# Kernel optimization log

Measured on AMD Instinct MI355X. Metric: run time of the kernel, lower is better.

Reference implementation:

```python
import jax, jax.numpy as jnp
import numpy as np

CROP = 20
HALF = CROP // 2  # also the zero-padding width
HID = 128
NCLS = 10
B = 16384


def setup_inputs() -> dict:
    key = jax.random.key(0)
    ks = jax.random.split(key, 16)
    s = 0.05
    inp = {
        "image": jax.random.uniform(ks[0], (B, 1, 28, 28), dtype=jnp.float32),
        # centers in padded coordinates, kept in-bounds: [HALF, 48-HALF]
        "center": jax.random.randint(ks[1], (B, 2), HALF, 48 - HALF + 1, dtype=jnp.int64),
        "h0": jax.random.normal(ks[2], (2, B, HID), dtype=jnp.float32),
        # RNN layer 0 (input 400 -> 128)
        "W_ih0": jax.random.normal(ks[3], (HID, CROP * CROP), dtype=jnp.float32) * s,
        "b_ih0": jax.random.normal(ks[4], (HID,), dtype=jnp.float32) * s,
        "W_hh0": jax.random.normal(ks[5], (HID, HID), dtype=jnp.float32) * s,
        "b_hh0": jax.random.normal(ks[6], (HID,), dtype=jnp.float32) * s,
        # RNN layer 1 (128 -> 128)
        "W_ih1": jax.random.normal(ks[7], (HID, HID), dtype=jnp.float32) * s,
        "b_ih1": jax.random.normal(ks[8], (HID,), dtype=jnp.float32) * s,
        "W_hh1": jax.random.normal(ks[9], (HID, HID), dtype=jnp.float32) * s,
        "b_hh1": jax.random.normal(ks[10], (HID,), dtype=jnp.float32) * s,
        # heads
        "W_cls": jax.random.normal(ks[11], (NCLS, HID), dtype=jnp.float32) * s,
        "b_cls": jax.random.normal(ks[12], (NCLS,), dtype=jnp.float32) * s,
        "W_act": jax.random.normal(ks[13], (2, HID), dtype=jnp.float32) * s,
        "b_act": jax.random.normal(ks[14], (2,), dtype=jnp.float32) * s,
    }
    return inp


def _crop(padded, center):
    # padded: (B,1,P,P), center: (B,2) with (x, y) in padded coords
    b = padded.shape[0]
    r = jnp.arange(CROP)
    ys = (center[:, 1] - HALF)[:, None] + r  # (B, CROP)
    xs = (center[:, 0] - HALF)[:, None] + r  # (B, CROP)
    bi = jnp.arange(b)[:, None, None]
    return padded[bi, 0, ys[:, :, None], xs[:, None, :]]  # (B, CROP, CROP)


def reference(image, center, h0,
              W_ih0, b_ih0, W_hh0, b_hh0,
              W_ih1, b_ih1, W_hh1, b_hh1,
              W_cls, b_cls, W_act, b_act):
    b = image.shape[0]
    padded = jnp.pad(image, ((0, 0), (0, 0), (HALF, HALF), (HALF, HALF)))
    x = _crop(padded, center).reshape(b, -1)  # (B, 400)
    # single-step, 2-layer tanh RNN
    h1 = jnp.tanh(x @ W_ih0.T + b_ih0 + h0[0] @ W_hh0.T + b_hh0)
    h2 = jnp.tanh(h1 @ W_ih1.T + b_ih1 + h0[1] @ W_hh1.T + b_hh1)
    hn = jnp.stack([h1, h2])  # (2, B, HID)
    class_pred = h2 @ W_cls.T + b_cls
    action_pred = h2 @ W_act.T + b_act
    return class_pred, action_pred, hn
```

## Files before the change

### kernel.cpp

```cpp
#include <hip/hip_runtime.h>
#include <hip/hip_bf16.h>

#define B_TOT 16384
#define MTILE 16

typedef __bf16 bf16x8 __attribute__((ext_vector_type(8)));
typedef float  f32x4  __attribute__((ext_vector_type(4)));

#define NG0 (17*8*64)
#define NG1 (8*8*64)
#define NGH (4*64)
#define WP0_OFF  0
#define WP1_OFF  (NG0*16)
#define WPH_OFF  (WP1_OFF + NG1*16)
#define BIAS0_OFF (WPH_OFF + NGH*16)
#define BIAS1_OFF (BIAS0_OFF + 512)
#define BIASH_OFF (BIAS1_OFF + 512)
#define PREP_BLOCKS 53

__device__ __forceinline__ float fast_tanh(float x) {
    float cx = fminf(fmaxf(x, -9.f), 9.f);
    float t = __builtin_amdgcn_exp2f(cx * 2.8853900817779268f);
    return 1.f - 2.f * __builtin_amdgcn_rcpf(t + 1.f);
}

__device__ __forceinline__ void gl_lds16(const void* g, void* l) {
    __builtin_amdgcn_global_load_lds((const __attribute__((address_space(1))) void*)g,
                                     (__attribute__((address_space(3))) void*)l, 16, 0, 0);
}

__device__ __forceinline__ bf16x8 cvt8(f32x4 a, f32x4 b) {
    bf16x8 v;
    v[0]=(__bf16)a.x; v[1]=(__bf16)a.y; v[2]=(__bf16)a.z; v[3]=(__bf16)a.w;
    v[4]=(__bf16)b.x; v[5]=(__bf16)b.y; v[6]=(__bf16)b.z; v[7]=(__bf16)b.w;
    return v;
}

__global__ __launch_bounds__(256) void prepack_kernel(
    const float* __restrict__ Wih0, const float* __restrict__ Whh0,
    const float* __restrict__ Wih1, const float* __restrict__ Whh1,
    const float* __restrict__ Wcls, const float* __restrict__ Wact,
    const float* __restrict__ bih0, const float* __restrict__ bhh0,
    const float* __restrict__ bih1, const float* __restrict__ bhh1,
    const float* __restrict__ bcls, const float* __restrict__ bact,
    char* __restrict__ ws)
{
    int idx = blockIdx.x * 256 + threadIdx.x;
    __bf16* wp0 = (__bf16*)(ws + WP0_OFF);
    __bf16* wp1 = (__bf16*)(ws + WP1_OFF);
    __bf16* wph = (__bf16*)(ws + WPH_OFF);
    float* bias0 = (float*)(ws + BIAS0_OFF);
    float* bias1 = (float*)(ws + BIAS1_OFF);
    float* biash = (float*)(ws + BIASH_OFF);

    if (idx < NG0) {
        int lane = idx & 63, g = idx >> 6, s = g >> 3, nb = g & 7;
        int n = nb * 16 + (lane & 15);
        int kb = s * 32 + (lane >> 4) * 8;
        bf16x8 v;
        #pragma unroll
        for (int j = 0; j < 8; ++j) {
            int k = kb + j;
            float x = 0.f;
            if (k < 400)       x = Wih0[n * 400 + k];
            else if (k >= 416) x = Whh0[n * 128 + (k - 416)];
            v[j] = (__bf16)x;
        }
        *(bf16x8*)(wp0 + (size_t)idx * 8) = v;
    } else if (idx < NG0 + NG1) {
        int i2 = idx - NG0;
        int lane = i2 & 63, g = i2 >> 6, s = g >> 3, nb = g & 7;
        int n = nb * 16 + (lane & 15);
        int kb = s * 32 + (lane >> 4) * 8;
        bf16x8 v;
        #pragma unroll
        for (int j = 0; j < 8; ++j) {
            int k = kb + j;
            float x = (k < 128) ? Wih1[n * 128 + k] : Whh1[n * 128 + (k - 128)];
            v[j] = (__bf16)x;
        }
        *(bf16x8*)(wp1 + (size_t)i2 * 8) = v;
    } else if (idx < NG0 + NG1 + NGH) {
        int i3 = idx - NG0 - NG1;
        int lane = i3 & 63, s = i3 >> 6;
        int n = lane & 15;
        int kb = s * 32 + (lane >> 4) * 8;
        bf16x8 v;
        #pragma unroll
        for (int j = 0; j < 8; ++j) {
            int k = kb + j;
            float x = 0.f;
            if (n < 10)      x = Wcls[n * 128 + k];
            else if (n < 12) x = Wact[(n - 10) * 128 + k];
            v[j] = (__bf16)x;
        }
        *(bf16x8*)(wph + (size_t)i3 * 8) = v;
    } else {
        int i4 = idx - NG0 - NG1 - NGH;
        if (i4 < 128) bias0[i4] = bih0[i4] + bhh0[i4];
        else if (i4 < 256) { int i = i4 - 128; bias1[i] = bih1[i] + bhh1[i]; }
        else if (i4 < 272) {
            int i = i4 - 256;
            biash[i] = (i < 10) ? bcls[i] : ((i < 12) ? bact[i - 10] : 0.f);
        }
    }
}

#define RAWW  560
#define XLSTR 424
#define HEXSTR 136

__global__ __launch_bounds__(256) void fused_main(
    const float* __restrict__ image, const int* __restrict__ center,
    const float* __restrict__ h0, const char* __restrict__ ws,
    float* __restrict__ out)
{
    const bf16x8* wp0 = (const bf16x8*)(ws + WP0_OFF);
    const bf16x8* wp1 = (const bf16x8*)(ws + WP1_OFF);
    const bf16x8* wph = (const bf16x8*)(ws + WPH_OFF);
    const float* bias0 = (const float*)(ws + BIAS0_OFF);
    const float* bias1 = (const float*)(ws + BIAS1_OFF);
    const float* biash = (const float*)(ws + BIASH_OFF);

    __shared__ __align__(16) float raw[MTILE * RAWW];
    __shared__ __align__(16) __bf16 stage[MTILE * XLSTR];
    __shared__ __align__(16) float h0st[8 * 256];
    __bf16* h1ex = (__bf16*)raw;
    __bf16* h2ex = (__bf16*)(raw + 2048);
    float*  h0st1 = raw + 4096;

    const int t = threadIdx.x, lane = t & 63, wn = t >> 6;
    const int m0 = blockIdx.x * MTILE;
    const int l15 = lane & 15, l16 = lane >> 4;

    #pragma unroll
    for (int u = 0; u < 2; ++u) {
        int c = wn * 2 + u;
        int s = c >> 1, half = c & 1;
        const float* src = h0 + (size_t)(m0 + l15) * 128 + s * 32 + l16 * 8 + half * 4;
        gl_lds16(src, &h0st[c * 256]);
    }

    {
        unsigned basel = lane * 16u;
        #pragma unroll
        for (int j = 0; j < 9; ++j) {
            int ii = wn + j * 4;
            if (ii < 35) {
                unsigned off = (unsigned)ii * 1024u + basel;
                unsigned sm = off / 2240u;
                unsigned within = off - sm * 2240u;
                int cyl = center[(m0 + sm) * 2 + 1];
                int rst = min(max(cyl - 20, 0), 8);
                const char* src = (const char*)image
                                + (size_t)(m0 + sm) * 3136 + (size_t)rst * 112 + within;
                gl_lds16(src, (char*)raw + (size_t)ii * 1024);
            }
        }
    }
    __syncthreads();

    {
        int m = t >> 4, sub = t & 15;
        int cyv = center[(m0 + m) * 2 + 1];
        int cxv = center[(m0 + m) * 2 + 0];
        int rst = min(max(cyv - 20, 0), 8);
        const float* rawm = raw + m * RAWW;
        __bf16* stm = stage + m * XLSTR;
        #pragma unroll
        for (int i = 0; i < 14; ++i) {
            int k2 = (sub + i * 16) * 2;
            if (k2 < XLSTR) {
                float v0 = 0.f, v1 = 0.f;
                if (k2 < 400) {
                    int r0 = k2 / 20, c0 = k2 - r0 * 20;
                    int iy = cyv - 20 + r0, ix = cxv - 20 + c0;
                    bool ok = ((unsigned)iy < 28u) && ((unsigned)ix < 28u);
                    int idx = ok ? ((iy - rst) * 28 + ix) : 0;
                    float vv = rawm[idx];
                    v0 = ok ? vv : 0.f;
                    int k1 = k2 + 1;
                    if (k1 < 400) {
                        int r1 = (c0 == 19) ? r0 + 1 : r0;
                        int c1 = (c0 == 19) ? 0 : c0 + 1;
                        int iy1 = cyv - 20 + r1, ix1 = cxv - 20 + c1;
                        bool ok1 = ((unsigned)iy1 < 28u) && ((unsigned)ix1 < 28u);
                        int idx1 = ok1 ? ((iy1 - rst) * 28 + ix1) : 0;
                        float vv1 = rawm[idx1];
                        v1 = ok1 ? vv1 : 0.f;
                    }
                }
                union { __bf16 b[2]; unsigned u; } p;
                p.b[0] = (__bf16)v0; p.b[1] = (__bf16)v1;
                *(unsigned*)(stm + k2) = p.u;
            }
        }
    }
    __syncthreads();

    #pragma unroll
    for (int u = 0; u < 2; ++u) {
        int c = wn * 2 + u;
        int s = c >> 1, half = c & 1;
        const float* src = h0 + (size_t)B_TOT * 128
                         + (size_t)(m0 + l15) * 128 + s * 32 + l16 * 8 + half * 4;
        gl_lds16(src, &h0st1[c * 256]);
    }

    const int cg = wn, qr = l16, lr = l15;
    float* outh1 = out + (size_t)B_TOT * 12;
    float* outh2 = out + (size_t)B_TOT * 140;

    f32x4 acc0[2] = {};
    {
        const __bf16* stg = stage + lr * XLSTR + qr * 8;
        #pragma unroll
        for (int s = 0; s < 13; ++s) {
            bf16x8 a = *(const bf16x8*)(stg + s * 32);
            bf16x8 b0 = wp0[(size_t)(s * 8 + cg * 2 + 0) * 64 + lane];
            bf16x8 b1 = wp0[(size_t)(s * 8 + cg * 2 + 1) * 64 + lane];
            acc0[0] = __builtin_amdgcn_mfma_f32_16x16x32_bf16(a, b0, acc0[0], 0, 0, 0);
            acc0[1] = __builtin_amdgcn_mfma_f32_16x16x32_bf16(a, b1, acc0[1], 0, 0, 0);
        }
    }
    #pragma unroll
    for (int s = 0; s < 4; ++s) {
        f32x4 fa = *(const f32x4*)(h0st + (s * 2 + 0) * 256 + lane * 4);
        f32x4 fb = *(const f32x4*)(h0st + (s * 2 + 1) * 256 + lane * 4);
        bf16x8 a = cvt8(fa, fb);
        bf16x8 b0 = wp0[(size_t)((13 + s) * 8 + cg * 2 + 0) * 64 + lane];
        bf16x8 b1 = wp0[(size_t)((13 + s) * 8 + cg * 2 + 1) * 64 + lane];
        acc0[0] = __builtin_amdgcn_mfma_f32_16x16x32_bf16(a, b0, acc0[0], 0, 0, 0);
        acc0[1] = __builtin_amdgcn_mfma_f32_16x16x32_bf16(a, b1, acc0[1], 0, 0, 0);
    }
    #pragma unroll
    for (int f = 0; f < 2; ++f) {
        int n = cg * 32 + f * 16 + lr;
        float bv = bias0[n];
        #pragma unroll
        for (int r = 0; r < 4; ++r) {
            int ml = qr * 4 + r;
            float hv = fast_tanh(acc0[f][r] + bv);
            outh1[(size_t)(m0 + ml) * 128 + n] = hv;
            h1ex[ml * HEXSTR + n] = (__bf16)hv;
        }
    }
    __syncthreads();

    f32x4 acc1[2] = {};
    {
        const __bf16* h1row = h1ex + lr * HEXSTR + qr * 8;
        #pragma unroll
        for (int s = 0; s < 4; ++s) {
            bf16x8 a  = *(const bf16x8*)(h1row + s * 32);
            bf16x8 b0 = wp1[(size_t)(s * 8 + cg * 2 + 0) * 64 + lane];
            bf16x8 b1 = wp1[(size_t)(s * 8 + cg * 2 + 1) * 64 + lane];
            acc1[0] = __builtin_amdgcn_mfma_f32_16x16x32_bf16(a, b0, acc1[0], 0, 0, 0);
            acc1[1] = __builtin_amdgcn_mfma_f32_16x16x32_bf16(a, b1, acc1[1], 0, 0, 0);
        }
    }
    #pragma unroll
    for (int s = 0; s < 4; ++s) {
        f32x4 fa = *(const f32x4*)(h0st1 + (s * 2 + 0) * 256 + lane * 4);
        f32x4 fb = *(const f32x4*)(h0st1 + (s * 2 + 1) * 256 + lane * 4);
        bf16x8 a = cvt8(fa, fb);
        bf16x8 b0 = wp1[(size_t)((4 + s) * 8 + cg * 2 + 0) * 64 + lane];
        bf16x8 b1 = wp1[(size_t)((4 + s) * 8 + cg * 2 + 1) * 64 + lane];
        acc1[0] = __builtin_amdgcn_mfma_f32_16x16x32_bf16(a, b0, acc1[0], 0, 0, 0);
        acc1[1] = __builtin_amdgcn_mfma_f32_16x16x32_bf16(a, b1, acc1[1], 0, 0, 0);
    }
    #pragma unroll
    for (int f = 0; f < 2; ++f) {
        int n = cg * 32 + f * 16 + lr;
        float bv = bias1[n];
        #pragma unroll
        for (int r = 0; r < 4; ++r) {
            int ml = qr * 4 + r;
            float hv = fast_tanh(acc1[f][r] + bv);
            outh2[(size_t)(m0 + ml) * 128 + n] = hv;
            h2ex[ml * HEXSTR + n] = (__bf16)hv;
        }
    }
    __syncthreads();

    if (cg == 0) {
        f32x4 acc2 = {};
        const __bf16* h2row = h2ex + lr * HEXSTR + qr * 8;
        #pragma unroll
        for (int s = 0; s < 4; ++s) {
            bf16x8 a = *(const bf16x8*)(h2row + s * 32);
            bf16x8 b = wph[(size_t)s * 64 + lane];
            acc2 = __builtin_amdgcn_mfma_f32_16x16x32_bf16(a, b, acc2, 0, 0, 0);
        }
        float bhd = biash[lr];
        #pragma unroll
        for (int r = 0; r < 4; ++r) {
            int mg = m0 + qr * 4 + r;
            float v = acc2[r] + bhd;
            if (lr < 10)      out[(size_t)mg * 10 + lr] = v;
            else if (lr < 12) out[(size_t)B_TOT * 10 + (size_t)mg * 2 + (lr - 10)] = v;
        }
    }
}

extern "C" void kernel_launch(void* const* d_in, const int* in_sizes, int n_in,
                              void* d_out, int out_size, void* d_ws, size_t ws_size,
                              hipStream_t stream) {
    const float* image = (const float*)d_in[0];
    const int*   center = (const int*)d_in[1];
    const float* h0   = (const float*)d_in[2];
    const float* Wih0 = (const float*)d_in[3];
    const float* bih0 = (const float*)d_in[4];
    const float* Whh0 = (const float*)d_in[5];
    const float* bhh0 = (const float*)d_in[6];
    const float* Wih1 = (const float*)d_in[7];
    const float* bih1 = (const float*)d_in[8];
    const float* Whh1 = (const float*)d_in[9];
    const float* bhh1 = (const float*)d_in[10];
    const float* Wcls = (const float*)d_in[11];
    const float* bcls = (const float*)d_in[12];
    const float* Wact = (const float*)d_in[13];
    const float* bact = (const float*)d_in[14];

    prepack_kernel<<<PREP_BLOCKS, 256, 0, stream>>>(
        Wih0, Whh0, Wih1, Whh1, Wcls, Wact,
        bih0, bhh0, bih1, bhh1, bcls, bact, (char*)d_ws);
    fused_main<<<B_TOT / MTILE, 256, 0, stream>>>(
        image, center, h0, (const char*)d_ws, (float*)d_out);
}
```

Baseline: 33.24 us.

## Load h0 directly from global and assign per-wave image rows for staging

Removes the LDS staging of both h0 layers and instead has each lane read its h0 fragment straight from global memory into registers right before the MFMA loops. The image-row prefetch is reorganized so each wave owns four samples, loads their centers once into registers, and issues contiguous 16-byte global-to-LDS copies per sample, with the crop/convert pass done by the same wave. This removes a shared array, the divide-based address math and repeated center loads, but exposes h0 global-load latency inside the compute path instead of overlapping it with the image load.

```diff
diff --git a/kernel.cpp b/kernel.cpp
--- a/kernel.cpp
+++ b/kernel.cpp
@@ -124,53 +124,42 @@
 
     __shared__ __align__(16) float raw[MTILE * RAWW];
     __shared__ __align__(16) __bf16 stage[MTILE * XLSTR];
-    __shared__ __align__(16) float h0st[8 * 256];
     __bf16* h1ex = (__bf16*)raw;
     __bf16* h2ex = (__bf16*)(raw + 2048);
-    float*  h0st1 = raw + 4096;
 
     const int t = threadIdx.x, lane = t & 63, wn = t >> 6;
     const int m0 = blockIdx.x * MTILE;
     const int l15 = lane & 15, l16 = lane >> 4;
-
-    #pragma unroll
-    for (int u = 0; u < 2; ++u) {
-        int c = wn * 2 + u;
-        int s = c >> 1, half = c & 1;
-        const float* src = h0 + (size_t)(m0 + l15) * 128 + s * 32 + l16 * 8 + half * 4;
-        gl_lds16(src, &h0st[c * 256]);
-    }
-
-    {
-        unsigned basel = lane * 16u;
-        #pragma unroll
-        for (int j = 0; j < 9; ++j) {
-            int ii = wn + j * 4;
-            if (ii < 35) {
-                unsigned off = (unsigned)ii * 1024u + basel;
-                unsigned sm = off / 2240u;
-                unsigned within = off - sm * 2240u;
-                int cyl = center[(m0 + sm) * 2 + 1];
-                int rst = min(max(cyl - 20, 0), 8);
-                const char* src = (const char*)image
-                                + (size_t)(m0 + sm) * 3136 + (size_t)rst * 112 + within;
-                gl_lds16(src, (char*)raw + (size_t)ii * 1024);
-            }
-        }
+    const int s0 = wn * 4;
+
+    int cxs[4], cys[4], rsts[4];
+    #pragma unroll
+    for (int i = 0; i < 4; ++i) {
+        cxs[i] = center[(m0 + s0 + i) * 2 + 0];
+        cys[i] = center[(m0 + s0 + i) * 2 + 1];
+        rsts[i] = min(max(cys[i] - 20, 0), 8);
+    }
+    #pragma unroll
+    for (int i = 0; i < 4; ++i) {
+        const char* src = (const char*)image + (size_t)(m0 + s0 + i) * 3136
+                        + (size_t)rsts[i] * 112;
+        char* dst = (char*)raw + (size_t)(s0 + i) * 2240;
+        gl_lds16(src + lane * 16, dst);
+        gl_lds16(src + 1024 + lane * 16, dst + 1024);
+        if (lane < 12) gl_lds16(src + 2048 + lane * 16, dst + 2048);
     }
     __syncthreads();
 
-    {
-        int m = t >> 4, sub = t & 15;
-        int cyv = center[(m0 + m) * 2 + 1];
-        int cxv = center[(m0 + m) * 2 + 0];
-        int rst = min(max(cyv - 20, 0), 8);
-        const float* rawm = raw + m * RAWW;
-        __bf16* stm = stage + m * XLSTR;
-        #pragma unroll
-        for (int i = 0; i < 14; ++i) {
-            int k2 = (sub + i * 16) * 2;
-            if (k2 < XLSTR) {
+    #pragma unroll
+    for (int i = 0; i < 4; ++i) {
+        const float* rawm = raw + (s0 + i) * RAWW;
+        __bf16* stm = stage + (s0 + i) * XLSTR;
+        const int cyv = cys[i], cxv = cxs[i], rst = rsts[i];
+        #pragma unroll
+        for (int j = 0; j < 4; ++j) {
+            int idx2 = lane + j * 64;
+            if (idx2 < 212) {
+                int k2 = idx2 * 2;
                 float v0 = 0.f, v1 = 0.f;
                 if (k2 < 400) {
                     int r0 = k2 / 20, c0 = k2 - r0 * 20;
@@ -198,16 +187,9 @@
     }
     __syncthreads();
 
-    #pragma unroll
-    for (int u = 0; u < 2; ++u) {
-        int c = wn * 2 + u;
-        int s = c >> 1, half = c & 1;
-        const float* src = h0 + (size_t)B_TOT * 128
-                         + (size_t)(m0 + l15) * 128 + s * 32 + l16 * 8 + half * 4;
-        gl_lds16(src, &h0st1[c * 256]);
-    }
-
     const int cg = wn, qr = l16, lr = l15;
+    const float* h0r0 = h0 + (size_t)(m0 + lr) * 128 + qr * 8;
+    const float* h0r1 = h0r0 + (size_t)B_TOT * 128;
     float* outh1 = out + (size_t)B_TOT * 12;
     float* outh2 = out + (size_t)B_TOT * 140;
 
@@ -225,8 +207,8 @@
     }
     #pragma unroll
     for (int s = 0; s < 4; ++s) {
-        f32x4 fa = *(const f32x4*)(h0st + (s * 2 + 0) * 256 + lane * 4);
-        f32x4 fb = *(const f32x4*)(h0st + (s * 2 + 1) * 256 + lane * 4);
+        f32x4 fa = *(const f32x4*)(h0r0 + s * 32);
+        f32x4 fb = *(const f32x4*)(h0r0 + s * 32 + 4);
         bf16x8 a = cvt8(fa, fb);
         bf16x8 b0 = wp0[(size_t)((13 + s) * 8 + cg * 2 + 0) * 64 + lane];
         bf16x8 b1 = wp0[(size_t)((13 + s) * 8 + cg * 2 + 1) * 64 + lane];
@@ -261,8 +243,8 @@
     }
     #pragma unroll
     for (int s = 0; s < 4; ++s) {
-        f32x4 fa = *(const f32x4*)(h0st1 + (s * 2 + 0) * 256 + lane * 4);
-        f32x4 fb = *(const f32x4*)(h0st1 + (s * 2 + 1) * 256 + lane * 4);
+        f32x4 fa = *(const f32x4*)(h0r1 + s * 32);
+        f32x4 fb = *(const f32x4*)(h0r1 + s * 32 + 4);
         bf16x8 a = cvt8(fa, fb);
         bf16x8 b0 = wp1[(size_t)((4 + s) * 8 + cg * 2 + 0) * 64 + lane];
         bf16x8 b1 = wp1[(size_t)((4 + s) * 8 + cg * 2 + 1) * 64 + lane];
```

Result: slower. 35.22 us (+6.0%).
